# Kernel optimization log

Hardware: AMD Instinct MI355X
Metric: run time of the kernel (lower is better)

Reference implementation:

```python
import jax, jax.numpy as jnp
import numpy as np
import math

ANGLE_THRESHOLD = math.radians(5.0)  # angle_threshold_deg=5.0
IQR_SCALE = 1.5
PI = np.pi


def setup_inputs() -> dict:
    key = jax.random.key(0)
    k1, k2 = jax.random.split(key)
    B, N, E = 1, 4096, 4096
    node_positions = jax.random.uniform(k1, (B, N, 2), dtype=jnp.float32) * 100.0
    adjacency = jnp.zeros((B, N, N), dtype=jnp.float32)  # unused by the axiom math
    edge_index = jax.random.randint(k2, (2, E), 0, B * N, dtype=jnp.int32)
    return {"node_positions": node_positions, "adjacency": adjacency, "edge_index": edge_index}


def reference(node_positions, adjacency, edge_index):
    """ParallelPairConstancyAxiom forward -> scalar loss.

    Vectorized equivalent of sort + host while-loop pair sweep: the pair set is
    exactly all (ei < ej) with circular angle distance <= threshold.
    """
    E = edge_index.shape[1]
    pos = node_positions.reshape(-1, 2)                      # (B*N, 2)
    src, dst = edge_index[0], edge_index[1]
    vec = pos[dst] - pos[src]                                # (E, 2)
    length = jnp.maximum(jnp.linalg.norm(vec, axis=-1, keepdims=True), 1e-8)
    dirs = vec / length                                      # normalized directions
    ang = jnp.arctan2(dirs[:, 1], dirs[:, 0]) % PI           # angles in [0, pi)

    # circular angle distance on [0, pi): min(|da|, pi-|da|)
    da = jnp.abs(ang[:, None] - ang[None, :])                # (E, E)
    circ = jnp.minimum(da, PI - da)
    upper = jnp.triu(jnp.ones((E, E), dtype=bool), k=1)      # ei < ej, no self-pairs
    mask = upper & (circ <= ANGLE_THRESHOLD)

    # perpendicular distance from edge i's line to midpoint of edge j
    normal = jnp.stack([-dirs[:, 1], dirs[:, 0]], axis=-1)   # (E, 2)
    mid = (pos[src] + pos[dst]) * 0.5                        # (E, 2)
    c = jnp.sum(pos[src] * normal, axis=-1)                  # (E,)
    dist = jnp.abs(normal @ mid.T - c[:, None])              # (E, E)

    n = jnp.sum(mask)                                        # number of parallel pairs
    sorted_d = jnp.sort(jnp.where(mask, dist, jnp.inf).reshape(-1))
    # torch: q1_idx = max(0, int(n*0.25)-1); q3_idx = min(n-1, int(n*0.75)); mu at n//2
    q1 = sorted_d[jnp.maximum(0, n // 4 - 1)]
    q3 = sorted_d[jnp.minimum(n - 1, (3 * n) // 4)]
    iqr = jnp.maximum(q3 - q1, 1e-6)
    mu = sorted_d[n // 2]
    margin = iqr * 0.5 * IQR_SCALE

    per_pair = jnp.maximum(jnp.abs(dist - mu) - margin, 0.0)
    loss = jnp.sum(jnp.where(mask, per_pair, 0.0)) / jnp.maximum(n, 1).astype(per_pair.dtype)
    return loss
```

## Files before the change

kernel.cpp:

```cpp
#include <hip/hip_runtime.h>
#include <hip/hip_bf16.h>
#include <math.h>

#define E_N 4096
#define PI_F 3.14159265358979323846f
#define ATH 0.08726646259971647f

#define AB_N 2048
#define AB_SCALE 651.8986469f
#define BWINP1 60

#define NB1 2048
#define SCALE1 12.8f
#define W1 0.078125f

#define NBLK2 32
#define THR2 1024
#define SUMSC 16384.0f
#define MASK44 ((1ull << 44) - 1ull)

#define O_A    0
#define O_B    65536
#define O_BST  131072
#define O_CTL  139264
#define O_H1   147456

__device__ __forceinline__ int bin_of(float a) {
    int b = (int)(a * AB_SCALE);
    return b < 0 ? 0 : (b > AB_N - 1 ? AB_N - 1 : b);
}

__global__ __launch_bounds__(1024) void init_sort(const void* __restrict__ posv,
                                                  const int* __restrict__ eidx,
                                                  char* __restrict__ ws)
{
    float4* A = (float4*)(ws + O_A);
    float4* B = (float4*)(ws + O_B);
    unsigned* bst = (unsigned*)(ws + O_BST);
    unsigned* ctl = (unsigned*)(ws + O_CTL);
    unsigned long long* h1 = (unsigned long long*)(ws + O_H1);

    __shared__ unsigned cnt[AB_N];
    __shared__ unsigned scn[1024];
    __shared__ unsigned flag;
    int tid = threadIdx.x;
    if (tid == 0) flag = 0u;
    if (tid < 64) ctl[tid] = 0u;
    h1[tid] = 0ull; h1[tid + 1024] = 0ull;
    cnt[tid] = 0u; cnt[tid + 1024] = 0u;
    __syncthreads();

    {
        const unsigned short* ph = (const unsigned short*)posv;
        unsigned f = 0;
#pragma unroll
        for (int k = 0; k < 8; ++k) {
            unsigned short v = ph[tid + k * 1024];
            if (((v >> 7) & 0xFFu) >= 137u) f = 1u;
        }
        if (f) atomicOr(&flag, 1u);
    }
    __syncthreads();
    bool isf32 = (flag != 0u);

    float rang[4], rnx[4], rny[4], rc[4], rmx[4], rmy[4];
    int lb[4];
#pragma unroll
    for (int k = 0; k < 4; ++k) {
        int e = tid + k * 1024;
        int s = eidx[e], d = eidx[E_N + e];
        float px, py, qx, qy;
        if (isf32) {
            const float* pf = (const float*)posv;
            px = pf[2*s]; py = pf[2*s+1]; qx = pf[2*d]; qy = pf[2*d+1];
        } else {
            const __hip_bfloat16* pb = (const __hip_bfloat16*)posv;
            px = __bfloat162float(pb[2*s]); py = __bfloat162float(pb[2*s+1]);
            qx = __bfloat162float(pb[2*d]); qy = __bfloat162float(pb[2*d+1]);
        }
        float vx = qx - px, vy = qy - py;
        float len = fmaxf(sqrtf(vx*vx + vy*vy), 1e-8f);
        float dx = vx / len, dy = vy / len;
        float a = fmodf(atan2f(dy, dx), PI_F);
        if (a < 0.0f) a += PI_F;
        rang[k] = a; rnx[k] = -dy; rny[k] = dx;
        rc[k]  = px * (-dy) + py * dx;
        rmx[k] = (px + qx) * 0.5f;
        rmy[k] = (py + qy) * 0.5f;
        lb[k] = bin_of(a);
        atomicAdd(&cnt[lb[k]], 1u);
    }
    __syncthreads();
    unsigned c0 = cnt[2*tid], c1 = cnt[2*tid+1], s2 = c0 + c1;
    scn[tid] = s2;
    __syncthreads();
    for (int off = 1; off < 1024; off <<= 1) {
        unsigned v = (tid >= off) ? scn[tid - off] : 0u;
        __syncthreads();
        scn[tid] += v;
        __syncthreads();
    }
    unsigned excl = scn[tid] - s2;
    bst[2*tid] = excl; bst[2*tid+1] = excl + c0;
    cnt[2*tid] = excl; cnt[2*tid+1] = excl + c0;
    __syncthreads();
#pragma unroll
    for (int k = 0; k < 4; ++k) {
        int e = tid + k * 1024;
        unsigned pos = atomicAdd(&cnt[lb[k]], 1u);
        unsigned eu = (unsigned)e;
        A[pos] = make_float4(rang[k], rmx[k], rmy[k], __uint_as_float(eu));
        B[pos] = make_float4(rnx[k], rny[k], rc[k], 0.0f);
    }
}

__global__ __launch_bounds__(THR2) void sweep(char* __restrict__ ws,
                                              unsigned* __restrict__ out)
{
    const float4* A = (const float4*)(ws + O_A);
    const float4* B = (const float4*)(ws + O_B);
    unsigned* bst = (unsigned*)(ws + O_BST);
    unsigned* ctl = (unsigned*)(ws + O_CTL);
    unsigned long long* h1 = (unsigned long long*)(ws + O_H1);

    __shared__ unsigned s_bst[AB_N];
    __shared__ unsigned long long s_s64[NB1];
    __shared__ float   s_vv[3];
    __shared__ float   s_lohi[2];
    __shared__ unsigned s_last;
    __shared__ double  s_dw[16];

    int tid = threadIdx.x, bid = blockIdx.x;
    int w = tid >> 6, lane = tid & 63;
    for (int k = tid; k < AB_N; k += THR2) s_bst[k] = bst[k];
    for (int k = tid; k < NB1; k += THR2) s_s64[k] = 0ull;
    __syncthreads();

#pragma unroll 1
    for (int i = 0; i < 8; ++i) {
        int p = bid * 128 + i * 16 + w;
        float4 pa = A[p];
        float4 pb = B[p];
        float ap = pa.x, pmx = pa.y, pmy = pa.z;
        unsigned op = __float_as_uint(pa.w);
        float pnx = pb.x, pny = pb.y, pc = pb.z;
        int bw = bin_of(ap) + BWINP1; if (bw >= AB_N) bw -= AB_N;
        unsigned wc = (s_bst[bw] + E_N - 1u - (unsigned)p) & (E_N - 1u);
#pragma unroll 1
        for (unsigned base = 0; base < wc; base += 64u) {
            unsigned t = base + lane;
            bool inb = t < wc;
            unsigned q = ((unsigned)p + 1u + t) & (E_N - 1u);
            float4 qa = A[q];
            float aq = qa.x;
            float df = aq - ap;
            float fa = (df >= 0.0f) ? df : df + PI_F;
            float da = fabsf(df);
            float circ = fminf(da, PI_F - da);
            bool own = (fa == 0.0f) ? (q > (unsigned)p) : (fa < 1.0f);
            if (inb && (circ <= ATH) && own) {
                unsigned oq = __float_as_uint(qa.w);
                float d;
                if (op < oq) {
                    d = fabsf(pnx * qa.y + pny * qa.z - pc);
                } else {
                    float4 qb = B[q];
                    d = fabsf(qb.x * pmx + qb.y * pmy - qb.z);
                }
                int b = (int)(d * SCALE1); if (b > NB1 - 1) b = NB1 - 1;
                atomicAdd(&s_s64[b],
                          (1ull << 44) | (unsigned long long)(d * SUMSC + 0.5f));
            }
        }
    }
    __syncthreads();
    for (int k = tid; k < NB1; k += THR2) {
        unsigned long long v = s_s64[k];
        if (v) atomicAdd(&h1[k], v);
    }
    __threadfence();
    __syncthreads();
    if (tid == 0) {
        unsigned tk = atomicAdd(&ctl[0], 1u);
        s_last = (tk == NBLK2 - 1u) ? 1u : 0u;
    }
    __syncthreads();
    if (!s_last) return;
    __threadfence();

    unsigned g0, g1; double S0, S1;
    {
        unsigned long long v0 = h1[2*tid], v1 = h1[2*tid+1];
        g0 = (unsigned)(v0 >> 44); g1 = (unsigned)(v1 >> 44);
        S0 = (double)(v0 & MASK44) * (1.0 / 16384.0);
        S1 = (double)(v1 & MASK44) * (1.0 / 16384.0);
    }
    unsigned gs = g0 + g1;
    s_bst[tid] = gs;
    __syncthreads();
    for (int off = 1; off < THR2; off <<= 1) {
        unsigned v = (tid >= off) ? s_bst[tid - off] : 0u;
        __syncthreads();
        s_bst[tid] += v;
        __syncthreads();
    }
    unsigned n = s_bst[THR2 - 1];
    if (n == 0) {
        if (tid == 0) {
            __hip_bfloat16 h = __float2bfloat16(0.0f);
            unsigned short b = *(unsigned short*)&h;
            out[0] = ((unsigned)b << 16) | (unsigned)b;
        }
        return;
    }
    long long q1i = (long long)(n / 4) - 1; if (q1i < 0) q1i = 0;
    long long q3i = (3LL * (long long)n) / 4;
    if (q3i > (long long)n - 1) q3i = (long long)n - 1;
    unsigned rks[3] = { (unsigned)q1i, n / 2, (unsigned)q3i };
    unsigned excl = s_bst[tid] - gs;
    unsigned gl[2] = { g0, g1 };
    for (int t = 0; t < 3; ++t) {
        unsigned r = rks[t];
        if (r >= excl && r < excl + gs) {
            unsigned cum = excl;
#pragma unroll
            for (int k = 0; k < 2; ++k) {
                unsigned c2 = cum + gl[k];
                if (r < c2) {
                    int b = 2 * tid + k;
                    float rr = (float)(r - cum);
                    s_vv[t] = ((float)b + (rr + 0.5f) / (float)gl[k]) * W1;
                    break;
                }
                cum = c2;
            }
        }
    }
    __syncthreads();
    if (tid == 0) {
        float iqr = fmaxf(s_vv[2] - s_vv[0], 1e-6f);
        float mu = s_vv[1];
        float margin = 0.75f * iqr;
        s_lohi[0] = mu - margin;
        s_lohi[1] = mu + margin;
    }
    __syncthreads();
    float lo = s_lohi[0], hi = s_lohi[1];
    double H = 0.0;
#pragma unroll
    for (int k = 0; k < 2; ++k) {
        int b = 2 * tid + k;
        unsigned c = gl[k];
        if (!c) continue;
        double S = k ? S1 : S0;
        float blo = (float)b * W1, bhi = blo + W1;
        if (bhi <= lo) {
            H += (double)lo * (double)c - S;
        } else if (blo >= hi) {
            H += S - (double)hi * (double)c;
        } else {
            double cf = (double)c / (double)W1;
            if (blo < lo) {
                float u1 = fminf(bhi, lo);
                double a0 = (double)lo - (double)blo;
                double a1 = (double)lo - (double)u1;
                H += cf * 0.5 * (a0 * a0 - a1 * a1);
            }
            if (bhi > hi) {
                float v0 = fmaxf(blo, hi);
                double b1 = (double)bhi - (double)hi;
                double b0 = (double)v0 - (double)hi;
                H += cf * 0.5 * (b1 * b1 - b0 * b0);
            }
        }
    }
    for (int off = 32; off > 0; off >>= 1) H += __shfl_down(H, off, 64);
    if (lane == 0) s_dw[w] = H;
    __syncthreads();
    if (tid == 0) {
        double tot = 0.0;
        for (int k = 0; k < THR2 / 64; ++k) tot += s_dw[k];
        float loss = (float)(tot / (double)n);
        __hip_bfloat16 h = __float2bfloat16(loss);
        unsigned short b = *(unsigned short*)&h;
        out[0] = ((unsigned)b << 16) | (unsigned)b;
    }
}

extern "C" void kernel_launch(void* const* d_in, const int* in_sizes, int n_in,
                              void* d_out, int out_size, void* d_ws, size_t ws_size,
                              hipStream_t stream) {
    const void* pos = d_in[0];
    const int* eidx = (const int*)d_in[2];
    char* ws = (char*)d_ws;
    unsigned* outp = (unsigned*)d_out;

    init_sort<<<1, 1024, 0, stream>>>(pos, eidx, ws);
    sweep<<<NBLK2, THR2, 0, stream>>>(ws, outp);
}
```

Measured before the change: 133.3 us.

## Replace sort-and-sweep with brute-force triangular tile pair histogram

Drops the single-block angle bucket sort and the windowed sweep. Instead it launches one block per upper-triangular 256x256 tile of edge pairs, recomputing edge geometry into shared memory and testing every pair directly. Global counters are zeroed with a memset rather than inside the init kernel. This trades the serial single-block sort stage for many more angle comparisons (all E^2/2 pairs) spread over 136 blocks, each of which also redoes the bf16/f32 input-format detection and geometry setup.

```diff
diff --git a/kernel.cpp b/kernel.cpp
--- a/kernel.cpp
+++ b/kernel.cpp
@@ -6,48 +6,47 @@
 #define PI_F 3.14159265358979323846f
 #define ATH 0.08726646259971647f
 
-#define AB_N 2048
-#define AB_SCALE 651.8986469f
-#define BWINP1 60
-
 #define NB1 2048
 #define SCALE1 12.8f
 #define W1 0.078125f
-
-#define NBLK2 32
-#define THR2 1024
 #define SUMSC 16384.0f
 #define MASK44 ((1ull << 44) - 1ull)
 
-#define O_A    0
-#define O_B    65536
-#define O_BST  131072
-#define O_CTL  139264
-#define O_H1   147456
-
-__device__ __forceinline__ int bin_of(float a) {
-    int b = (int)(a * AB_SCALE);
-    return b < 0 ? 0 : (b > AB_N - 1 ? AB_N - 1 : b);
-}
-
-__global__ __launch_bounds__(1024) void init_sort(const void* __restrict__ posv,
-                                                  const int* __restrict__ eidx,
-                                                  char* __restrict__ ws)
+#define TILE 256
+#define NT   (E_N / TILE)
+#define NBLK (NT * (NT + 1) / 2)
+#define THR  1024
+
+#define O_CTL 0
+#define O_H1  64
+#define ZBYTES (O_H1 + NB1 * 8)
+
+__global__ __launch_bounds__(THR) void pair_hist(const void* __restrict__ posv,
+                                                 const int* __restrict__ eidx,
+                                                 char* __restrict__ ws,
+                                                 unsigned* __restrict__ out)
 {
-    float4* A = (float4*)(ws + O_A);
-    float4* B = (float4*)(ws + O_B);
-    unsigned* bst = (unsigned*)(ws + O_BST);
     unsigned* ctl = (unsigned*)(ws + O_CTL);
     unsigned long long* h1 = (unsigned long long*)(ws + O_H1);
 
-    __shared__ unsigned cnt[AB_N];
-    __shared__ unsigned scn[1024];
-    __shared__ unsigned flag;
-    int tid = threadIdx.x;
-    if (tid == 0) flag = 0u;
-    if (tid < 64) ctl[tid] = 0u;
-    h1[tid] = 0ull; h1[tid + 1024] = 0ull;
-    cnt[tid] = 0u; cnt[tid + 1024] = 0u;
+    __shared__ float4 rowA[TILE];
+    __shared__ float4 colA[TILE];
+    __shared__ unsigned long long s_s64[NB1];
+    __shared__ unsigned s_scan[THR];
+    __shared__ float   s_vv[3];
+    __shared__ float   s_lohi[2];
+    __shared__ unsigned s_last;
+    __shared__ double  s_dw[THR / 64];
+    __shared__ unsigned s_flag;
+
+    int tid = threadIdx.x, bid = blockIdx.x;
+
+    int tr = 0, rem = bid;
+    while (rem >= NT - tr) { rem -= NT - tr; ++tr; }
+    int tc = tr + rem;
+
+    if (tid == 0) s_flag = 0u;
+    for (int k = tid; k < NB1; k += THR) s_s64[k] = 0ull;
     __syncthreads();
 
     {
@@ -58,115 +57,51 @@
             unsigned short v = ph[tid + k * 1024];
             if (((v >> 7) & 0xFFu) >= 137u) f = 1u;
         }
-        if (f) atomicOr(&flag, 1u);
-    }
-    __syncthreads();
-    bool isf32 = (flag != 0u);
-
-    float rang[4], rnx[4], rny[4], rc[4], rmx[4], rmy[4];
-    int lb[4];
-#pragma unroll
-    for (int k = 0; k < 4; ++k) {
-        int e = tid + k * 1024;
-        int s = eidx[e], d = eidx[E_N + e];
+        if (f) atomicOr(&s_flag, 1u);
+    }
+    __syncthreads();
+    bool isf32 = (s_flag != 0u);
+
+    if (tid < 2 * TILE) {
+        bool isCol = tid < TILE;
+        int local = isCol ? tid : tid - TILE;
+        int e = (isCol ? tc : tr) * TILE + local;
+        int s = eidx[e], d2 = eidx[E_N + e];
         float px, py, qx, qy;
         if (isf32) {
             const float* pf = (const float*)posv;
-            px = pf[2*s]; py = pf[2*s+1]; qx = pf[2*d]; qy = pf[2*d+1];
+            px = pf[2*s]; py = pf[2*s+1]; qx = pf[2*d2]; qy = pf[2*d2+1];
         } else {
             const __hip_bfloat16* pb = (const __hip_bfloat16*)posv;
             px = __bfloat162float(pb[2*s]); py = __bfloat162float(pb[2*s+1]);
-            qx = __bfloat162float(pb[2*d]); qy = __bfloat162float(pb[2*d+1]);
+            qx = __bfloat162float(pb[2*d2]); qy = __bfloat162float(pb[2*d2+1]);
         }
         float vx = qx - px, vy = qy - py;
         float len = fmaxf(sqrtf(vx*vx + vy*vy), 1e-8f);
         float dx = vx / len, dy = vy / len;
         float a = fmodf(atan2f(dy, dx), PI_F);
         if (a < 0.0f) a += PI_F;
-        rang[k] = a; rnx[k] = -dy; rny[k] = dx;
-        rc[k]  = px * (-dy) + py * dx;
-        rmx[k] = (px + qx) * 0.5f;
-        rmy[k] = (py + qy) * 0.5f;
-        lb[k] = bin_of(a);
-        atomicAdd(&cnt[lb[k]], 1u);
-    }
-    __syncthreads();
-    unsigned c0 = cnt[2*tid], c1 = cnt[2*tid+1], s2 = c0 + c1;
-    scn[tid] = s2;
-    __syncthreads();
-    for (int off = 1; off < 1024; off <<= 1) {
-        unsigned v = (tid >= off) ? scn[tid - off] : 0u;
-        __syncthreads();
-        scn[tid] += v;
-        __syncthreads();
-    }
-    unsigned excl = scn[tid] - s2;
-    bst[2*tid] = excl; bst[2*tid+1] = excl + c0;
-    cnt[2*tid] = excl; cnt[2*tid+1] = excl + c0;
-    __syncthreads();
-#pragma unroll
-    for (int k = 0; k < 4; ++k) {
-        int e = tid + k * 1024;
-        unsigned pos = atomicAdd(&cnt[lb[k]], 1u);
-        unsigned eu = (unsigned)e;
-        A[pos] = make_float4(rang[k], rmx[k], rmy[k], __uint_as_float(eu));
-        B[pos] = make_float4(rnx[k], rny[k], rc[k], 0.0f);
-    }
-}
-
-__global__ __launch_bounds__(THR2) void sweep(char* __restrict__ ws,
-                                              unsigned* __restrict__ out)
-{
-    const float4* A = (const float4*)(ws + O_A);
-    const float4* B = (const float4*)(ws + O_B);
-    unsigned* bst = (unsigned*)(ws + O_BST);
-    unsigned* ctl = (unsigned*)(ws + O_CTL);
-    unsigned long long* h1 = (unsigned long long*)(ws + O_H1);
-
-    __shared__ unsigned s_bst[AB_N];
-    __shared__ unsigned long long s_s64[NB1];
-    __shared__ float   s_vv[3];
-    __shared__ float   s_lohi[2];
-    __shared__ unsigned s_last;
-    __shared__ double  s_dw[16];
-
-    int tid = threadIdx.x, bid = blockIdx.x;
-    int w = tid >> 6, lane = tid & 63;
-    for (int k = tid; k < AB_N; k += THR2) s_bst[k] = bst[k];
-    for (int k = tid; k < NB1; k += THR2) s_s64[k] = 0ull;
-    __syncthreads();
-
-#pragma unroll 1
-    for (int i = 0; i < 8; ++i) {
-        int p = bid * 128 + i * 16 + w;
-        float4 pa = A[p];
-        float4 pb = B[p];
-        float ap = pa.x, pmx = pa.y, pmy = pa.z;
-        unsigned op = __float_as_uint(pa.w);
-        float pnx = pb.x, pny = pb.y, pc = pb.z;
-        int bw = bin_of(ap) + BWINP1; if (bw >= AB_N) bw -= AB_N;
-        unsigned wc = (s_bst[bw] + E_N - 1u - (unsigned)p) & (E_N - 1u);
-#pragma unroll 1
-        for (unsigned base = 0; base < wc; base += 64u) {
-            unsigned t = base + lane;
-            bool inb = t < wc;
-            unsigned q = ((unsigned)p + 1u + t) & (E_N - 1u);
-            float4 qa = A[q];
-            float aq = qa.x;
-            float df = aq - ap;
-            float fa = (df >= 0.0f) ? df : df + PI_F;
-            float da = fabsf(df);
+        if (isCol) colA[local] = make_float4(a, (px + qx) * 0.5f, (py + qy) * 0.5f, 0.0f);
+        else       rowA[local] = make_float4(a, -dy, dx, px * (-dy) + py * dx);
+    }
+    __syncthreads();
+
+    {
+        int r = tid & (TILE - 1);
+        int q = tid >> 8;
+        float4 rg = rowA[r];
+        float angp = rg.x, nx = rg.y, ny = rg.z, c = rg.w;
+        int j0 = q * 64;
+        bool diag = (tr == tc);
+#pragma unroll 4
+        for (int jj = 0; jj < 64; ++jj) {
+            int j = j0 + jj;
+            if (diag && j <= r) continue;
+            float4 cg = colA[j];
+            float da = fabsf(angp - cg.x);
             float circ = fminf(da, PI_F - da);
-            bool own = (fa == 0.0f) ? (q > (unsigned)p) : (fa < 1.0f);
-            if (inb && (circ <= ATH) && own) {
-                unsigned oq = __float_as_uint(qa.w);
-                float d;
-                if (op < oq) {
-                    d = fabsf(pnx * qa.y + pny * qa.z - pc);
-                } else {
-                    float4 qb = B[q];
-                    d = fabsf(qb.x * pmx + qb.y * pmy - qb.z);
-                }
+            if (circ <= ATH) {
+                float d = fabsf(nx * cg.y + ny * cg.z - c);
                 int b = (int)(d * SCALE1); if (b > NB1 - 1) b = NB1 - 1;
                 atomicAdd(&s_s64[b],
                           (1ull << 44) | (unsigned long long)(d * SUMSC + 0.5f));
@@ -174,7 +109,8 @@
         }
     }
     __syncthreads();
-    for (int k = tid; k < NB1; k += THR2) {
+
+    for (int k = tid; k < NB1; k += THR) {
         unsigned long long v = s_s64[k];
         if (v) atomicAdd(&h1[k], v);
     }
@@ -182,12 +118,13 @@
     __syncthreads();
     if (tid == 0) {
         unsigned tk = atomicAdd(&ctl[0], 1u);
-        s_last = (tk == NBLK2 - 1u) ? 1u : 0u;
+        s_last = (tk == NBLK - 1u) ? 1u : 0u;
     }
     __syncthreads();
     if (!s_last) return;
     __threadfence();
 
+    int w = tid >> 6, lane = tid & 63;
     unsigned g0, g1; double S0, S1;
     {
         unsigned long long v0 = h1[2*tid], v1 = h1[2*tid+1];
@@ -196,15 +133,15 @@
         S1 = (double)(v1 & MASK44) * (1.0 / 16384.0);
     }
     unsigned gs = g0 + g1;
-    s_bst[tid] = gs;
-    __syncthreads();
-    for (int off = 1; off < THR2; off <<= 1) {
-        unsigned v = (tid >= off) ? s_bst[tid - off] : 0u;
+    s_scan[tid] = gs;
+    __syncthreads();
+    for (int off = 1; off < THR; off <<= 1) {
+        unsigned v = (tid >= off) ? s_scan[tid - off] : 0u;
         __syncthreads();
-        s_bst[tid] += v;
+        s_scan[tid] += v;
         __syncthreads();
     }
-    unsigned n = s_bst[THR2 - 1];
+    unsigned n = s_scan[THR - 1];
     if (n == 0) {
         if (tid == 0) {
             __hip_bfloat16 h = __float2bfloat16(0.0f);
@@ -217,7 +154,7 @@
     long long q3i = (3LL * (long long)n) / 4;
     if (q3i > (long long)n - 1) q3i = (long long)n - 1;
     unsigned rks[3] = { (unsigned)q1i, n / 2, (unsigned)q3i };
-    unsigned excl = s_bst[tid] - gs;
+    unsigned excl = s_scan[tid] - gs;
     unsigned gl[2] = { g0, g1 };
     for (int t = 0; t < 3; ++t) {
         unsigned r = rks[t];
@@ -279,7 +216,7 @@
     __syncthreads();
     if (tid == 0) {
         double tot = 0.0;
-        for (int k = 0; k < THR2 / 64; ++k) tot += s_dw[k];
+        for (int k = 0; k < THR / 64; ++k) tot += s_dw[k];
         float loss = (float)(tot / (double)n);
         __hip_bfloat16 h = __float2bfloat16(loss);
         unsigned short b = *(unsigned short*)&h;
@@ -295,6 +232,6 @@
     char* ws = (char*)d_ws;
     unsigned* outp = (unsigned*)d_out;
 
-    init_sort<<<1, 1024, 0, stream>>>(pos, eidx, ws);
-    sweep<<<NBLK2, THR2, 0, stream>>>(ws, outp);
+    hipMemsetAsync(ws, 0, ZBYTES, stream);
+    pair_hist<<<NBLK, THR, 0, stream>>>(pos, eidx, ws, outp);
 }
```

Measured after the change: 141.8 us. 6.4% more time.
